# Optimization experiments

Hardware: AMD Instinct MI355X
Metric: run time of the kernel (lower is better)

Reference implementation:

```python
import jax, jax.numpy as jnp
import numpy as np


def setup_inputs() -> dict:
    key = jax.random.key(0)
    k1, k2, k3, k4, k5 = jax.random.split(key, 5)
    T, R, K, D = 8, 512, 4, 4096          # tiles, rows/tile, group size, in_features
    N_CW = 16384                           # codebook size
    N_TOK = 512                            # tokens
    x = jax.random.normal(k1, (N_TOK, D), dtype=jnp.float32)
    codewords = jax.random.normal(k2, (N_CW, D), dtype=jnp.float32) * 0.02
    indices = jax.random.randint(k3, (T, R, K), 0, N_CW, dtype=jnp.int64)
    rotations = jax.random.normal(k4, (T, D, D), dtype=jnp.float32) * (1.0 / np.sqrt(D))
    scales = jax.random.uniform(k5, (T,), dtype=jnp.float32) + 0.5
    bias = jnp.zeros((D,), dtype=jnp.float32)
    return {"x": x, "codewords": codewords, "indices": indices,
            "rotations": rotations, "scales": scales, "bias": bias}


def reference(x, codewords, indices, rotations, scales, bias):
    # Decode weight tiles: gather [T,R,K,D] -> mean over group -> [T,R,D]
    decoded = codewords[indices].mean(axis=2)
    # Per-tile rotation and scale: [T,R,D] @ [T,D,D] -> [T,R,D]
    decoded = jnp.einsum('trd,tde->tre', decoded, rotations) * scales[:, None, None]
    T, R, D = decoded.shape
    weight = decoded.reshape(T * R, D)     # [out_features, in_features]
    # Linear: x @ W^T + b
    return x @ weight.T + bias
```

## Files before the change

### kernel.cpp

```cpp
#include <hip/hip_runtime.h>

typedef unsigned int uint32;
typedef unsigned short u16;
typedef float fx4 __attribute__((ext_vector_type(4)));
typedef uint32 u32x4 __attribute__((ext_vector_type(4)));
typedef uint32 u32x2 __attribute__((ext_vector_type(2)));

typedef const __attribute__((address_space(1))) void gvoid;
typedef __attribute__((address_space(3))) void lvoid;

#define MFMA_BF16_16x16x32(acc, a, b) \
  asm("v_mfma_f32_16x16x32_bf16 %0, %1, %2, %0" : "+v"(acc) : "v"(a), "v"(b))

#define WAIT_LGKM0() asm volatile("s_waitcnt lgkmcnt(0)" ::: "memory")
#define WAIT_LGKM2() asm volatile("s_waitcnt lgkmcnt(2)" ::: "memory")
#define WAIT_LGKM6() asm volatile("s_waitcnt lgkmcnt(6)" ::: "memory")
#define WAIT_VM0()   asm volatile("s_waitcnt vmcnt(0)" ::: "memory")
#define WAIT_VM3()   asm volatile("s_waitcnt vmcnt(3)" ::: "memory")
#define WAIT_VM4()   asm volatile("s_waitcnt vmcnt(4)" ::: "memory")
#define WAIT_VM8()   asm volatile("s_waitcnt vmcnt(8)" ::: "memory")
#define WAIT_VM12()  asm volatile("s_waitcnt vmcnt(12)" ::: "memory")
#define SFENCE()     __builtin_amdgcn_sched_barrier(0)
#define BARRIER()    do { __builtin_amdgcn_s_barrier(); asm volatile("" ::: "memory"); } while (0)

__device__ __forceinline__ u16 f2bf_rne(float f) {
  uint32 u = __builtin_bit_cast(uint32, f);
  u += 0x7FFFu + ((u >> 16) & 1u);
  return (u16)(u >> 16);
}

__device__ __forceinline__ uint32 cvt_pk_bf16(float lo, float hi) {
  uint32 r;
  asm("v_cvt_pk_bf16_f32 %0, %1, %2" : "=v"(r) : "v"(lo), "v"(hi));
  return r;
}

__global__ __launch_bounds__(256) void cvtx_kernel(const float* __restrict__ x,
                                                   u16* __restrict__ xb) {
  const int i = blockIdx.x * 256 + threadIdx.x;
  float4 v = ((const float4*)x)[i];
  ushort4 o;
  o.x = f2bf_rne(v.x);
  o.y = f2bf_rne(v.y);
  o.z = f2bf_rne(v.z);
  o.w = f2bf_rne(v.w);
  ((ushort4*)xb)[i] = o;
}

__device__ __forceinline__ void decode_body(
    int bid, const float* __restrict__ cw, const int* __restrict__ indices,
    const float* __restrict__ scales, u16* __restrict__ dec) {
  const int tid = threadIdx.x;
#pragma unroll 1
  for (int rr = 0; rr < 16; ++rr) {
    const int row = bid * 16 + rr;
    const int t = row >> 9;
    const int* ip = indices + (size_t)row * 4;
    const float* c0 = cw + (size_t)ip[0] * 4096;
    const float* c1 = cw + (size_t)ip[1] * 4096;
    const float* c2 = cw + (size_t)ip[2] * 4096;
    const float* c3 = cw + (size_t)ip[3] * 4096;
    const float s = scales[t] * 0.25f;
    u16* orow = dec + (size_t)row * 4096;
#pragma unroll
    for (int j = 0; j < 4; ++j) {
      const int d = j * 1024 + tid * 4;
      float4 a = *(const float4*)(c0 + d);
      float4 b = *(const float4*)(c1 + d);
      float4 c = *(const float4*)(c2 + d);
      float4 e = *(const float4*)(c3 + d);
      ushort4 o;
      o.x = f2bf_rne((a.x + b.x + c.x + e.x) * s);
      o.y = f2bf_rne((a.y + b.y + c.y + e.y) * s);
      o.z = f2bf_rne((a.z + b.z + c.z + e.z) * s);
      o.w = f2bf_rne((a.w + b.w + c.w + e.w) * s);
      *(ushort4*)(orow + d) = o;
    }
  }
}

__global__ __launch_bounds__(256, 2) void fused_z_decode_kernel(
    const u16* __restrict__ Xb,
    const float* __restrict__ rot,
    u16* __restrict__ Z,
    const float* __restrict__ cw, const int* __restrict__ indices,
    const float* __restrict__ scales, u16* __restrict__ dec) {
  __shared__ char sA[32768];
  __shared__ char sB[32768];

  const int bid = blockIdx.x;
  if (bid < 256) {
    decode_body(bid, cw, indices, scales, dec);
    return;
  }
  const int lb = bid - 256;
  const int swz = ((lb & 7) << 7) | (lb >> 3);
  const int t = swz >> 7;
  const int rem = swz & 127;
  const int nb = rem >> 2, mb = rem & 3;
  const float* Bt = rot + ((size_t)t << 24);
  u16* Ct = Z + ((size_t)t << 21);
  const int aRow0 = mb << 7, bCol0 = nb << 7;
  const int tid = threadIdx.x;
  const int wv = tid >> 6, ln = tid & 63;
  const int lr = ln & 15, lk = ln >> 4;
  const int wr = wv >> 1, wc = wv & 1;

  fx4 acc[4][4] = {};

  const u16* Asrc = Xb + (size_t)(aRow0 + (ln >> 2)) * 4096 +
                    (((ln & 3) ^ ((ln >> 3) & 3)) << 3);
  const int R0 = wv * 32 + (ln >> 3);
  const int cB = ln & 7;
  const float* Bsrc = Bt + (size_t)(bCol0 + R0) * 4096 + cB * 4;
  const int bwr = R0 * 64 + ((((cB >> 1) ^ ((R0 >> 1) & 3)) << 4)) + ((cB & 1) << 3);
  const int gr = (lr >> 1) & 3;
  const int aof = (wr * 64 + lr) * 64 + ((lk ^ gr) << 4);
  const int bof = (wc * 64 + lr) * 64 + ((lk ^ gr) << 4);

#define STAGE_A_Z(dbuf, kofs)                                                 \
  _Pragma("unroll")                                                           \
  for (int c = 0; c < 4; ++c)                                                 \
    __builtin_amdgcn_global_load_lds(                                         \
        (gvoid*)(Asrc + (size_t)(((c & 1) * 4 + wv) << 4) * 4096 +            \
                 ((c >> 1) << 5) + (kofs)),                                   \
        (lvoid*)(sA + (dbuf) * 16384 + c * 4096 + tid * 16), 16, 0, 0)

#define LOADB4(p, kofs, Q)                                                    \
  do {                                                                        \
    const float* bp_ = Bsrc + (kofs) + (Q) * 32;                              \
    p[(Q) * 4 + 0] = *(const float4*)(bp_);                                   \
    p[(Q) * 4 + 1] = *(const float4*)(bp_ + 8 * 4096);                        \
    p[(Q) * 4 + 2] = *(const float4*)(bp_ + 16 * 4096);                       \
    p[(Q) * 4 + 3] = *(const float4*)(bp_ + 24 * 4096);                       \
  } while (0)

#define PACK_B(p, dst)                                                        \
  do {                                                                        \
    u32x2 w_;                                                                 \
    w_[0] = cvt_pk_bf16(p[0].x, p[0].y); w_[1] = cvt_pk_bf16(p[0].z, p[0].w); \
    *(u32x2*)((dst) + bwr) = w_;                                              \
    w_[0] = cvt_pk_bf16(p[1].x, p[1].y); w_[1] = cvt_pk_bf16(p[1].z, p[1].w); \
    *(u32x2*)((dst) + bwr + 512) = w_;                                        \
    w_[0] = cvt_pk_bf16(p[2].x, p[2].y); w_[1] = cvt_pk_bf16(p[2].z, p[2].w); \
    *(u32x2*)((dst) + bwr + 1024) = w_;                                       \
    w_[0] = cvt_pk_bf16(p[3].x, p[3].y); w_[1] = cvt_pk_bf16(p[3].z, p[3].w); \
    *(u32x2*)((dst) + bwr + 1536) = w_;                                       \
    w_[0] = cvt_pk_bf16(p[4].x, p[4].y); w_[1] = cvt_pk_bf16(p[4].z, p[4].w); \
    *(u32x2*)((dst) + 8192 + bwr) = w_;                                       \
    w_[0] = cvt_pk_bf16(p[5].x, p[5].y); w_[1] = cvt_pk_bf16(p[5].z, p[5].w); \
    *(u32x2*)((dst) + 8192 + bwr + 512) = w_;                                 \
    w_[0] = cvt_pk_bf16(p[6].x, p[6].y); w_[1] = cvt_pk_bf16(p[6].z, p[6].w); \
    *(u32x2*)((dst) + 8192 + bwr + 1024) = w_;                                \
    w_[0] = cvt_pk_bf16(p[7].x, p[7].y); w_[1] = cvt_pk_bf16(p[7].z, p[7].w); \
    *(u32x2*)((dst) + 8192 + bwr + 1536) = w_;                                \
  } while (0)

#define PH_READS0(d)                                                          \
  do {                                                                        \
    const char* pA_ = sA + (d) * 16384;                                       \
    const char* pB_ = sB + (d) * 16384;                                       \
    af0[0] = *(const u32x4*)(pA_ + aof);                                      \
    af0[1] = *(const u32x4*)(pA_ + aof + 1024);                               \
    af0[2] = *(const u32x4*)(pA_ + aof + 2048);                               \
    af0[3] = *(const u32x4*)(pA_ + aof + 3072);                               \
    bf0[0] = *(const u32x4*)(pB_ + bof);                                      \
    bf0[1] = *(const u32x4*)(pB_ + bof + 1024);                               \
  } while (0)
#define PH_READS1(d)                                                          \
  do {                                                                        \
    const char* pB_ = sB + (d) * 16384;                                       \
    bf0[2] = *(const u32x4*)(pB_ + bof + 2048);                               \
    bf0[3] = *(const u32x4*)(pB_ + bof + 3072);                               \
  } while (0)
#define PH_READS2(d)                                                          \
  do {                                                                        \
    const char* pA_ = sA + (d) * 16384 + 8192;                                \
    const char* pB_ = sB + (d) * 16384 + 8192;                                \
    af1[0] = *(const u32x4*)(pA_ + aof);                                      \
    af1[1] = *(const u32x4*)(pA_ + aof + 1024);                               \
    af1[2] = *(const u32x4*)(pA_ + aof + 2048);                               \
    af1[3] = *(const u32x4*)(pA_ + aof + 3072);                               \
    bf1[0] = *(const u32x4*)(pB_ + bof);                                      \
    bf1[1] = *(const u32x4*)(pB_ + bof + 1024);                               \
  } while (0)
#define PH_READS3(d)                                                          \
  do {                                                                        \
    const char* pB_ = sB + (d) * 16384 + 8192;                                \
    bf1[2] = *(const u32x4*)(pB_ + bof + 2048);                               \
    bf1[3] = *(const u32x4*)(pB_ + bof + 3072);                               \
  } while (0)

#define MFMA_PH(AF, BF, NA, NB)                                               \
  do {                                                                        \
    __builtin_amdgcn_s_setprio(1);                                            \
    _Pragma("unroll")                                                         \
    for (int m = 0; m < 4; ++m) {                                             \
      MFMA_BF16_16x16x32(acc[m][NA], AF[m], BF[NA]);                          \
      MFMA_BF16_16x16x32(acc[m][NB], AF[m], BF[NB]);                          \
    }                                                                         \
    __builtin_amdgcn_s_setprio(0);                                            \
  } while (0)

  u32x4 af0[4], af1[4], bf0[4], bf1[4];
  float4 pa[8], pb[8];

  STAGE_A_Z(0, 0);
  LOADB4(pa, 0, 0);
  LOADB4(pa, 0, 1);
  WAIT_VM0();
  PACK_B(pa, sB);
  LOADB4(pb, 64, 0);
  LOADB4(pb, 64, 1);
  WAIT_LGKM0();
  BARRIER();

#pragma unroll 1
  for (int kt2 = 0; kt2 < 62; kt2 += 2) {
    PH_READS0(0);
    STAGE_A_Z(1, (kt2 + 1) << 6);
    PH_READS1(0);
    WAIT_LGKM2();
    SFENCE();
    MFMA_PH(af0, bf0, 0, 1);
    LOADB4(pa, (kt2 + 2) << 6, 0);
    PH_READS2(0);
    WAIT_LGKM6();
    SFENCE();
    MFMA_PH(af0, bf0, 2, 3);
    LOADB4(pa, (kt2 + 2) << 6, 1);
    PH_READS3(0);
    WAIT_LGKM2();
    SFENCE();
    MFMA_PH(af1, bf1, 0, 1);
    WAIT_LGKM0();
    SFENCE();
    MFMA_PH(af1, bf1, 2, 3);
    WAIT_VM12();
    PACK_B(pb, sB + 16384);
    WAIT_VM8();
    WAIT_LGKM0();
    BARRIER();
    PH_READS0(1);
    STAGE_A_Z(0, (kt2 + 2) << 6);
    PH_READS1(1);
    WAIT_LGKM2();
    SFENCE();
    MFMA_PH(af0, bf0, 0, 1);
    LOADB4(pb, (kt2 + 3) << 6, 0);
    PH_READS2(1);
    WAIT_LGKM6();
    SFENCE();
    MFMA_PH(af0, bf0, 2, 3);
    LOADB4(pb, (kt2 + 3) << 6, 1);
    PH_READS3(1);
    WAIT_LGKM2();
    SFENCE();
    MFMA_PH(af1, bf1, 0, 1);
    WAIT_LGKM0();
    SFENCE();
    MFMA_PH(af1, bf1, 2, 3);
    WAIT_VM12();
    PACK_B(pa, sB);
    WAIT_VM8();
    WAIT_LGKM0();
    BARRIER();
  }
  {
    PH_READS0(0);
    STAGE_A_Z(1, 63 << 6);
    PH_READS1(0);
    WAIT_LGKM2();
    SFENCE();
    MFMA_PH(af0, bf0, 0, 1);
    PH_READS2(0);
    WAIT_LGKM6();
    SFENCE();
    MFMA_PH(af0, bf0, 2, 3);
    PH_READS3(0);
    WAIT_LGKM2();
    SFENCE();
    MFMA_PH(af1, bf1, 0, 1);
    WAIT_LGKM0();
    SFENCE();
    MFMA_PH(af1, bf1, 2, 3);
    WAIT_VM4();
    PACK_B(pb, sB + 16384);
    WAIT_VM0();
    WAIT_LGKM0();
    BARRIER();
  }
  {
    PH_READS0(1);
    PH_READS1(1);
    WAIT_LGKM2();
    SFENCE();
    MFMA_PH(af0, bf0, 0, 1);
    PH_READS2(1);
    WAIT_LGKM6();
    SFENCE();
    MFMA_PH(af0, bf0, 2, 3);
    PH_READS3(1);
    WAIT_LGKM2();
    SFENCE();
    MFMA_PH(af1, bf1, 0, 1);
    WAIT_LGKM0();
    SFENCE();
    MFMA_PH(af1, bf1, 2, 3);
  }

#pragma unroll
  for (int m = 0; m < 4; ++m) {
    const int r0 = aRow0 + wr * 64 + m * 16 + lk * 4;
#pragma unroll
    for (int n = 0; n < 4; ++n) {
      const int col = bCol0 + wc * 64 + n * 16 + lr;
#pragma unroll
      for (int j = 0; j < 4; ++j)
        Ct[(size_t)(r0 + j) * 4096 + col] = f2bf_rne(acc[m][n][j]);
    }
  }
#undef STAGE_A_Z
#undef LOADB4
#undef PACK_B
#undef PH_READS0
#undef PH_READS1
#undef PH_READS2
#undef PH_READS3
#undef MFMA_PH
}

__global__ __launch_bounds__(256, 2) void gemm_out_kernel(
    const u16* __restrict__ Z,
    const u16* __restrict__ Dec,
    const float* __restrict__ bias,
    float* __restrict__ out) {
  __shared__ char sm[36864];
  const int lb = blockIdx.x;
  const int swz = ((lb & 7) << 5) | (lb >> 3);
  const int t = swz >> 5;
  const int rem = swz & 31;
  const int nb = rem >> 2, mb = rem & 3;
  const u16* At = Z + ((size_t)t << 21);
  const u16* Bt = Dec + ((size_t)t << 21);
  const int aRow0 = mb << 7, bCol0 = nb << 6;
  const int tid = threadIdx.x;
  const int wv = tid >> 6, ln = tid & 63;
  const int lr = ln & 15, lk = ln >> 4;
  const int wr = wv >> 1, wc = wv & 1;

  fx4 acc[4][2] = {};

  const int kswz = (((tid & 3) ^ ((tid >> 3) & 3)) << 3);
  const u16* Asrc = At + (size_t)(aRow0 + (tid >> 2)) * 4096 + kswz;
  const u16* Bsrc = Bt + (size_t)(bCol0 + (tid >> 2)) * 4096 + kswz;
  const int gr = (lr >> 1) & 3;
  const int aof = (wr * 64 + lr) * 64 + ((lk ^ gr) << 4);
  const int bof = 8192 + (wc * 32 + lr) * 64 + ((lk ^ gr) << 4);

#define STAGE_O(buf, kofs)                                                   \
  do {                                                                       \
    _Pragma("unroll")                                                        \
    for (int c = 0; c < 2; ++c)                                              \
      __builtin_amdgcn_global_load_lds(                                      \
          (gvoid*)(Asrc + (size_t)(c << 6) * 4096 + (kofs)),                 \
          (lvoid*)((buf) + c * 4096 + tid * 16), 16, 0, 0);                  \
    __builtin_amdgcn_global_load_lds((gvoid*)(Bsrc + (kofs)),                \
                                     (lvoid*)((buf) + 8192 + tid * 16), 16,  \
                                     0, 0);                                  \
  } while (0)

  char* b0 = sm;
  char* b1 = sm + 12288;
  char* b2 = sm + 24576;
  STAGE_O(b0, 0);
  STAGE_O(b1, 32);
  WAIT_VM3();
  BARRIER();

#pragma unroll 1
  for (int kt = 0; kt < 128; ++kt) {
    if (kt + 2 < 128) STAGE_O(b2, (kt + 2) << 5);
    u32x4 af[4], bf[2];
#pragma unroll
    for (int m = 0; m < 4; ++m)
      af[m] = *(const u32x4*)(b0 + aof + m * 1024);
#pragma unroll
    for (int n = 0; n < 2; ++n)
      bf[n] = *(const u32x4*)(b0 + bof + n * 1024);
    WAIT_LGKM0();
    SFENCE();
#pragma unroll
    for (int m = 0; m < 4; ++m)
#pragma unroll
      for (int n = 0; n < 2; ++n)
        MFMA_BF16_16x16x32(acc[m][n], af[m], bf[n]);
    if (kt + 2 < 128) {
      WAIT_VM3();
    } else {
      WAIT_VM0();
    }
    BARRIER();
    char* tmp = b0; b0 = b1; b1 = b2; b2 = tmp;
  }

#pragma unroll
  for (int n = 0; n < 2; ++n) {
    const int colg = (t << 9) + bCol0 + wc * 32 + n * 16 + lr;
    const float bv = bias[colg];
#pragma unroll
    for (int m = 0; m < 4; ++m) {
      const int r0 = aRow0 + wr * 64 + m * 16 + lk * 4;
#pragma unroll
      for (int j = 0; j < 4; ++j)
        out[(size_t)(r0 + j) * 4096 + colg] = acc[m][n][j] + bv;
    }
  }
#undef STAGE_O
}

extern "C" void kernel_launch(void* const* d_in, const int* in_sizes, int n_in,
                              void* d_out, int out_size, void* d_ws, size_t ws_size,
                              hipStream_t stream) {
  const float* x       = (const float*)d_in[0];
  const float* cw      = (const float*)d_in[1];
  const int*   indices = (const int*)d_in[2];
  const float* rot     = (const float*)d_in[3];
  const float* scales  = (const float*)d_in[4];
  const float* bias    = (const float*)d_in[5];
  float* out = (float*)d_out;
  char* ws = (char*)d_ws;

  u16* xb  = (u16*)(ws);
  u16* dec = (u16*)(ws + ((size_t)4 << 20));
  u16* z   = (u16*)(ws + ((size_t)36 << 20));

  cvtx_kernel<<<dim3(2048), dim3(256), 0, stream>>>(x, xb);
  fused_z_decode_kernel<<<dim3(1280), dim3(256), 0, stream>>>(
      xb, rot, z, cw, indices, scales, dec);
  gemm_out_kernel<<<dim3(256), dim3(256), 0, stream>>>(z, dec, bias, out);
}
```

Before: 316.0 us.

## Deepen global-load prefetch pipelines in decode and output GEMM kernels

The decode/rotation GEMM now keeps three register sets of fp32 B loads in flight, prefetching four k-steps ahead instead of two. Its main loop is restructured into a 6-step unrolled macro with explicit scheduling fences, and the B packing moves to the end of each step. The output GEMM goes from a 3-stage to a 4-stage LDS ring buffer, raising shared memory to 48KB per block. The aim is to hide global memory latency. The cost is more VGPR pressure in the first kernel and more LDS in the second, which may lower occupancy under the 2-blocks launch bound.

```diff
diff --git a/kernel.cpp b/kernel.cpp
--- a/kernel.cpp
+++ b/kernel.cpp
@@ -17,9 +17,9 @@
 #define WAIT_LGKM6() asm volatile("s_waitcnt lgkmcnt(6)" ::: "memory")
 #define WAIT_VM0()   asm volatile("s_waitcnt vmcnt(0)" ::: "memory")
 #define WAIT_VM3()   asm volatile("s_waitcnt vmcnt(3)" ::: "memory")
-#define WAIT_VM4()   asm volatile("s_waitcnt vmcnt(4)" ::: "memory")
+#define WAIT_VM6()   asm volatile("s_waitcnt vmcnt(6)" ::: "memory")
 #define WAIT_VM8()   asm volatile("s_waitcnt vmcnt(8)" ::: "memory")
-#define WAIT_VM12()  asm volatile("s_waitcnt vmcnt(12)" ::: "memory")
+#define WAIT_VM16()  asm volatile("s_waitcnt vmcnt(16)" ::: "memory")
 #define SFENCE()     __builtin_amdgcn_sched_barrier(0)
 #define BARRIER()    do { __builtin_amdgcn_s_barrier(); asm volatile("" ::: "memory"); } while (0)
 
@@ -202,105 +202,92 @@
     __builtin_amdgcn_s_setprio(0);                                            \
   } while (0)
 
+#define STEP_Z(d, SET, kt, DOLOAD, DOSTAGE, TAILW)                            \
+  do {                                                                        \
+    PH_READS0(d);                                                             \
+    SFENCE();                                                                 \
+    if (DOSTAGE) { STAGE_A_Z((d) ^ 1, ((kt) + 1) << 6); }                     \
+    SFENCE();                                                                 \
+    PH_READS1(d);                                                             \
+    SFENCE();                                                                 \
+    WAIT_LGKM2();                                                             \
+    SFENCE();                                                                 \
+    MFMA_PH(af0, bf0, 0, 1);                                                  \
+    PH_READS2(d);                                                             \
+    SFENCE();                                                                 \
+    WAIT_LGKM6();                                                             \
+    SFENCE();                                                                 \
+    MFMA_PH(af0, bf0, 2, 3);                                                  \
+    PH_READS3(d);                                                             \
+    SFENCE();                                                                 \
+    WAIT_LGKM2();                                                             \
+    SFENCE();                                                                 \
+    MFMA_PH(af1, bf1, 0, 1);                                                  \
+    WAIT_LGKM0();                                                             \
+    SFENCE();                                                                 \
+    MFMA_PH(af1, bf1, 2, 3);                                                  \
+    PACK_B(SET, sB + ((d) ^ 1) * 16384);                                      \
+    SFENCE();                                                                 \
+    if (DOLOAD) { LOADB4(SET, ((kt) + 4) << 6, 0);                            \
+                  LOADB4(SET, ((kt) + 4) << 6, 1); }                          \
+    SFENCE();                                                                 \
+    TAILW;                                                                    \
+    WAIT_LGKM0();                                                             \
+    BARRIER();                                                                \
+  } while (0)
+
   u32x4 af0[4], af1[4], bf0[4], bf1[4];
-  float4 pa[8], pb[8];
+  float4 pa[8], pb[8], pc[8];
 
   STAGE_A_Z(0, 0);
+  SFENCE();
   LOADB4(pa, 0, 0);
   LOADB4(pa, 0, 1);
+  SFENCE();
   WAIT_VM0();
+  SFENCE();
   PACK_B(pa, sB);
-  LOADB4(pb, 64, 0);
-  LOADB4(pb, 64, 1);
+  SFENCE();
+  LOADB4(pb, 1 << 6, 0);
+  LOADB4(pb, 1 << 6, 1);
+  SFENCE();
+  LOADB4(pc, 2 << 6, 0);
+  LOADB4(pc, 2 << 6, 1);
+  SFENCE();
+  LOADB4(pa, 3 << 6, 0);
+  LOADB4(pa, 3 << 6, 1);
+  SFENCE();
+  WAIT_VM16();
   WAIT_LGKM0();
   BARRIER();
 
 #pragma unroll 1
-  for (int kt2 = 0; kt2 < 62; kt2 += 2) {
-    PH_READS0(0);
-    STAGE_A_Z(1, (kt2 + 1) << 6);
-    PH_READS1(0);
-    WAIT_LGKM2();
-    SFENCE();
-    MFMA_PH(af0, bf0, 0, 1);
-    LOADB4(pa, (kt2 + 2) << 6, 0);
-    PH_READS2(0);
-    WAIT_LGKM6();
-    SFENCE();
-    MFMA_PH(af0, bf0, 2, 3);
-    LOADB4(pa, (kt2 + 2) << 6, 1);
-    PH_READS3(0);
-    WAIT_LGKM2();
-    SFENCE();
-    MFMA_PH(af1, bf1, 0, 1);
-    WAIT_LGKM0();
-    SFENCE();
-    MFMA_PH(af1, bf1, 2, 3);
-    WAIT_VM12();
-    PACK_B(pb, sB + 16384);
-    WAIT_VM8();
-    WAIT_LGKM0();
-    BARRIER();
-    PH_READS0(1);
-    STAGE_A_Z(0, (kt2 + 2) << 6);
-    PH_READS1(1);
-    WAIT_LGKM2();
-    SFENCE();
-    MFMA_PH(af0, bf0, 0, 1);
-    LOADB4(pb, (kt2 + 3) << 6, 0);
-    PH_READS2(1);
-    WAIT_LGKM6();
-    SFENCE();
-    MFMA_PH(af0, bf0, 2, 3);
-    LOADB4(pb, (kt2 + 3) << 6, 1);
-    PH_READS3(1);
-    WAIT_LGKM2();
-    SFENCE();
-    MFMA_PH(af1, bf1, 0, 1);
-    WAIT_LGKM0();
-    SFENCE();
-    MFMA_PH(af1, bf1, 2, 3);
-    WAIT_VM12();
-    PACK_B(pa, sB);
-    WAIT_VM8();
-    WAIT_LGKM0();
-    BARRIER();
-  }
-  {
-    PH_READS0(0);
-    STAGE_A_Z(1, 63 << 6);
-    PH_READS1(0);
-    WAIT_LGKM2();
-    SFENCE();
-    MFMA_PH(af0, bf0, 0, 1);
-    PH_READS2(0);
-    WAIT_LGKM6();
-    SFENCE();
-    MFMA_PH(af0, bf0, 2, 3);
-    PH_READS3(0);
-    WAIT_LGKM2();
-    SFENCE();
-    MFMA_PH(af1, bf1, 0, 1);
-    WAIT_LGKM0();
-    SFENCE();
-    MFMA_PH(af1, bf1, 2, 3);
-    WAIT_VM4();
-    PACK_B(pb, sB + 16384);
-    WAIT_VM0();
-    WAIT_LGKM0();
-    BARRIER();
-  }
+  for (int kt6 = 0; kt6 < 60; kt6 += 6) {
+    STEP_Z(0, pb, kt6 + 0, true, true, WAIT_VM8());
+    STEP_Z(1, pc, kt6 + 1, true, true, WAIT_VM8());
+    STEP_Z(0, pa, kt6 + 2, true, true, WAIT_VM8());
+    STEP_Z(1, pb, kt6 + 3, true, true, WAIT_VM8());
+    STEP_Z(0, pc, kt6 + 4, true, true, WAIT_VM8());
+    STEP_Z(1, pa, kt6 + 5, true, true, WAIT_VM8());
+  }
+  STEP_Z(0, pb, 60, false, true, WAIT_VM0());
+  STEP_Z(1, pc, 61, false, true, WAIT_VM0());
+  STEP_Z(0, pa, 62, false, true, WAIT_VM0());
   {
     PH_READS0(1);
+    SFENCE();
     PH_READS1(1);
+    SFENCE();
     WAIT_LGKM2();
     SFENCE();
     MFMA_PH(af0, bf0, 0, 1);
     PH_READS2(1);
+    SFENCE();
     WAIT_LGKM6();
     SFENCE();
     MFMA_PH(af0, bf0, 2, 3);
     PH_READS3(1);
+    SFENCE();
     WAIT_LGKM2();
     SFENCE();
     MFMA_PH(af1, bf1, 0, 1);
@@ -328,6 +315,7 @@
 #undef PH_READS2
 #undef PH_READS3
 #undef MFMA_PH
+#undef STEP_Z
 }
 
 __global__ __launch_bounds__(256, 2) void gemm_out_kernel(
@@ -335,7 +323,7 @@
     const u16* __restrict__ Dec,
     const float* __restrict__ bias,
     float* __restrict__ out) {
-  __shared__ char sm[36864];
+  __shared__ char sm[49152];
   const int lb = blockIdx.x;
   const int swz = ((lb & 7) << 5) | (lb >> 3);
   const int t = swz >> 5;
@@ -373,14 +361,16 @@
   char* b0 = sm;
   char* b1 = sm + 12288;
   char* b2 = sm + 24576;
+  char* b3 = sm + 36864;
   STAGE_O(b0, 0);
   STAGE_O(b1, 32);
-  WAIT_VM3();
+  STAGE_O(b2, 64);
+  WAIT_VM6();
   BARRIER();
 
 #pragma unroll 1
   for (int kt = 0; kt < 128; ++kt) {
-    if (kt + 2 < 128) STAGE_O(b2, (kt + 2) << 5);
+    if (kt + 3 < 128) STAGE_O(b3, (kt + 3) << 5);
     u32x4 af[4], bf[2];
 #pragma unroll
     for (int m = 0; m < 4; ++m)
@@ -395,13 +385,15 @@
 #pragma unroll
       for (int n = 0; n < 2; ++n)
         MFMA_BF16_16x16x32(acc[m][n], af[m], bf[n]);
-    if (kt + 2 < 128) {
+    if (kt + 3 < 128) {
+      WAIT_VM6();
+    } else if (kt + 2 < 128) {
       WAIT_VM3();
     } else {
       WAIT_VM0();
     }
     BARRIER();
-    char* tmp = b0; b0 = b1; b1 = b2; b2 = tmp;
+    char* tmp = b0; b0 = b1; b1 = b2; b2 = b3; b3 = tmp;
   }
 
 #pragma unroll
```

After: 298.5 us. 1.06x faster.
